# Performance work log

Hardware: AMD Instinct MI355X
Metric: run time of the kernel (lower is better)

Reference implementation:

```python
import jax, jax.numpy as jnp
import numpy as np

EPS = 1e-12  # F.normalize default eps

def _l1_normalize(x, axis):
    return x / jnp.maximum(jnp.sum(jnp.abs(x), axis=axis, keepdims=True), EPS)


def setup_inputs() -> dict:
    key = jax.random.key(0)
    k1, k2, k3, k4 = jax.random.split(key, 4)
    B_src, S_src, d = 4096, 32, 512
    B_tgt, T = 32, 256
    m = jax.random.normal(k1, (B_src, S_src, d), dtype=jnp.float32)
    om = jax.random.normal(k2, (B_tgt, T, d), dtype=jnp.float32)
    src_mask = jax.random.randint(k3, (B_src, 1, S_src), 0, 2, dtype=jnp.int32)
    tgt_mask = jax.random.randint(k4, (B_tgt, T, T), 0, 2, dtype=jnp.int32)
    return {"m": m, "om": om, "src_mask": src_mask, "tgt_mask": tgt_mask}


def reference(m, om, src_mask, tgt_mask):
    # masked mean readouts (L1-normalized masks as attention weights)
    src_w = _l1_normalize(src_mask.astype(jnp.float32), axis=-1)      # [B_src,1,S_src]
    src_readout = jnp.einsum('bos,bsd->bod', src_w, m)[:, 0, :]       # [B_src,d]
    tgt_w = _l1_normalize(tgt_mask.astype(jnp.float32), axis=-1)      # [B_tgt,T,T]
    tgt_readout = jnp.einsum('btu,bud->btd', tgt_w, om)               # [B_tgt,T,d]

    # pairwise L2 distance over d WITHOUT materializing [B_tgt,T,B_src,d]:
    # ||t - s||^2 = ||t||^2 + ||s||^2 - 2 t.s
    t_sq = jnp.sum(tgt_readout * tgt_readout, axis=-1)                # [B_tgt,T]
    s_sq = jnp.sum(src_readout * src_readout, axis=-1)                # [B_src]
    cross = jnp.einsum('btd,nd->btn', tgt_readout, src_readout)       # [B_tgt,T,B_src]
    d2 = t_sq[..., None] + s_sq[None, None, :] - 2.0 * cross
    dist = jnp.sqrt(jnp.maximum(d2, EPS))
    sim = jnp.exp(-dist)
    sim = _l1_normalize(sim, axis=-1)                                 # [B_tgt,T,B_src]
    return sim
```

## Files before the change

### kernel.cpp

```cpp
#include <hip/hip_runtime.h>
#include <math.h>

#define EPSF 1e-12f

typedef short bf16x8 __attribute__((ext_vector_type(8)));
typedef float f32x4 __attribute__((ext_vector_type(4)));

__device__ __forceinline__ void gload_lds16(const void* g, void* l) {
  __builtin_amdgcn_global_load_lds(
      (const __attribute__((address_space(1))) unsigned int*)g,
      (__attribute__((address_space(3))) unsigned int*)l, 16, 0, 0);
}

__device__ __forceinline__ unsigned short bf16_rne(float f) {
  unsigned int u = __float_as_uint(f);
  u += 0x7fffu + ((u >> 16) & 1u);
  return (unsigned short)(u >> 16);
}

__device__ __forceinline__ float bf16_to_f32(unsigned short h) {
  return __uint_as_float((unsigned int)h << 16);
}

__device__ __forceinline__ float block_reduce_sum_256(float v) {
#pragma unroll
  for (int o = 32; o > 0; o >>= 1) v += __shfl_down(v, o, 64);
  __shared__ float ws4[4];
  const int lane = threadIdx.x & 63;
  const int w = threadIdx.x >> 6;
  if (lane == 0) ws4[w] = v;
  __syncthreads();
  if (threadIdx.x == 0) ws4[0] = ws4[0] + ws4[1] + ws4[2] + ws4[3];
  __syncthreads();
  return ws4[0];
}

__global__ __launch_bounds__(256) void k_src_readout(const float* __restrict__ m,
                                                     const int* __restrict__ src_mask,
                                                     unsigned short* __restrict__ srcRb,
                                                     float* __restrict__ ssq) {
  const int tid = threadIdx.x;
  const int sub = tid >> 7, t = tid & 127;
  const int b = blockIdx.x * 2 + sub;
  __shared__ int msk[2][32];
  __shared__ float sinv[2];
  __shared__ float red[4];
  if (t < 32) msk[sub][t] = src_mask[b * 32 + t];
  __syncthreads();
  if (t == 0) {
    float c = 0.f;
    for (int s = 0; s < 32; ++s) c += (float)msk[sub][s];
    sinv[sub] = 1.0f / fmaxf(c, EPSF);
  }
  __syncthreads();
  const float inv = sinv[sub];
  const float4* mb = (const float4*)(m + (size_t)b * (32 * 512)) + t;
  float ax = 0.f, ay = 0.f, az = 0.f, aw = 0.f;
  for (int s = 0; s < 32; ++s) {
    if (msk[sub][s] != 0) {
      float4 v = mb[s * 128];
      ax += v.x; ay += v.y; az += v.z; aw += v.w;
    }
  }
  ushort4 o;
  o.x = bf16_rne(ax * inv);
  o.y = bf16_rne(ay * inv);
  o.z = bf16_rne(az * inv);
  o.w = bf16_rne(aw * inv);
  *(ushort4*)(srcRb + (size_t)b * 512 + t * 4) = o;
  float fx = bf16_to_f32(o.x), fy = bf16_to_f32(o.y);
  float fz = bf16_to_f32(o.z), fw = bf16_to_f32(o.w);
  float s = fx * fx + fy * fy + fz * fz + fw * fw;
#pragma unroll
  for (int oo = 32; oo > 0; oo >>= 1) s += __shfl_down(s, oo, 64);
  if ((tid & 63) == 0) red[tid >> 6] = s;
  __syncthreads();
  if (t == 0) ssq[b] = red[sub * 2] + red[sub * 2 + 1];
}

#define WST 72
__global__ __launch_bounds__(512) void k_tgt_readout_mfma(
    const float* __restrict__ om, const int* __restrict__ tgt_mask,
    unsigned short* __restrict__ Afrag) {
  const int b = blockIdx.x, dq = blockIdx.y, th = blockIdx.z;
  const int d0 = dq * 128, t0 = th * 128;
  __shared__ unsigned short Wb[128 * WST];
  __shared__ unsigned short omT[128 * WST];
  __shared__ float cntp[128 * 4];
  __shared__ float cnt_inv[128];
  const int tid = threadIdx.x;
  const int lane = tid & 63, w = tid >> 6;
  const int* mbase = tgt_mask + (size_t)b * 65536 + (size_t)t0 * 256;

  {
    const int t = tid >> 2, q = tid & 3;
    const int* mp = mbase + t * 256 + q * 64;
    int c = 0;
#pragma unroll
    for (int k = 0; k < 16; ++k) {
      int4 v = *(const int4*)(mp + 4 * k);
      c += v.x + v.y + v.z + v.w;
    }
    cntp[t * 4 + q] = (float)c;
  }
  __syncthreads();
  if (tid < 128) {
    float c = cntp[tid * 4] + cntp[tid * 4 + 1] + cntp[tid * 4 + 2] + cntp[tid * 4 + 3];
    cnt_inv[tid] = 1.0f / fmaxf(c, EPSF);
  }

  f32x4 acc[8];
#pragma unroll
  for (int di = 0; di < 8; ++di) acc[di] = (f32x4){0.f, 0.f, 0.f, 0.f};

  for (int uc = 0; uc < 4; ++uc) {
    const int ub = uc * 64;
    __syncthreads();
    {
      const int t = tid >> 2, ul0 = (tid & 3) * 16;
      const int* mp = mbase + t * 256 + ub + ul0;
      unsigned short* wp = Wb + t * WST + ul0;
#pragma unroll
      for (int k = 0; k < 4; ++k) {
        int4 v = *(const int4*)(mp + 4 * k);
        ushort4 h;
        h.x = v.x ? 0x3F80 : 0;
        h.y = v.y ? 0x3F80 : 0;
        h.z = v.z ? 0x3F80 : 0;
        h.w = v.w ? 0x3F80 : 0;
        *(ushort4*)(wp + 4 * k) = h;
      }
    }
    {
#pragma unroll
      for (int k = 0; k < 4; ++k) {
        const int idx = tid + 512 * k;
        const int u = idx >> 5, dl = (idx & 31) * 4;
        float4 v = *(const float4*)(om + (size_t)b * 131072 + (size_t)(ub + u) * 512 + d0 + dl);
        omT[(dl + 0) * WST + u] = bf16_rne(v.x);
        omT[(dl + 1) * WST + u] = bf16_rne(v.y);
        omT[(dl + 2) * WST + u] = bf16_rne(v.z);
        omT[(dl + 3) * WST + u] = bf16_rne(v.w);
      }
    }
    __syncthreads();
#pragma unroll
    for (int kt2 = 0; kt2 < 2; ++kt2) {
      const int ko = kt2 * 32 + (lane >> 4) * 8;
      bf16x8 wf = *(const bf16x8*)(Wb + (w * 16 + (lane & 15)) * WST + ko);
      bf16x8 of[8];
#pragma unroll
      for (int di = 0; di < 8; ++di)
        of[di] = *(const bf16x8*)(omT + (di * 16 + (lane & 15)) * WST + ko);
#pragma unroll
      for (int di = 0; di < 8; ++di)
        acc[di] = __builtin_amdgcn_mfma_f32_16x16x32_bf16(of[di], wf, acc[di], 0, 0, 0);
    }
  }

  const int tl = w * 16 + (lane & 15);
  const int rT = b * 256 + t0 + tl;
  const float inv = cnt_inv[tl];
#pragma unroll
  for (int di = 0; di < 8; ++di) {
    const int d = d0 + di * 16 + (lane >> 4) * 4;
    ushort4 o;
    o.x = bf16_rne(acc[di][0] * inv);
    o.y = bf16_rne(acc[di][1] * inv);
    o.z = bf16_rne(acc[di][2] * inv);
    o.w = bf16_rne(acc[di][3] * inv);
    const size_t off =
        (((size_t)(rT >> 4) * 16 + (d >> 5)) * 64 + ((d >> 3) & 3) * 16 + (rT & 15)) * 8 + (d & 7);
    *(ushort4*)(Afrag + off) = o;
  }
}

__global__ __launch_bounds__(256) void k_rowsq_frag(const unsigned short* __restrict__ Afrag,
                                                    float* __restrict__ sq) {
  const int r = blockIdx.x;
  const int tid = threadIdx.x;
  const int g = r >> 4, rl = r & 15;
  const int d = 2 * tid;
  const size_t off = ((size_t)((g * 16 + (d >> 5)) * 64 + ((d >> 3) & 3) * 16 + rl)) * 8 + (d & 7);
  ushort2 v = *(const ushort2*)(Afrag + off);
  float fx = bf16_to_f32(v.x), fy = bf16_to_f32(v.y);
  float s = fx * fx + fy * fy;
  s = block_reduce_sum_256(s);
  if (tid == 0) sq[r] = s;
}

template <int BF16SIM>
__global__ __launch_bounds__(512, 2) void k_cross_mfma(
    const unsigned short* __restrict__ Afrag, const unsigned short* __restrict__ B,
    const float* __restrict__ tsq, const float* __restrict__ ssq,
    unsigned short* __restrict__ simU, float* __restrict__ psum,
    float* __restrict__ outF) {
  __shared__ unsigned short Bs[128 * 512];
  const int tid = threadIdx.x;
  const int lane = tid & 63, w = tid >> 6;
  const int bid = blockIdx.x;
  const int xcd = bid & 7, idx = bid >> 3;
  const int row0 = (xcd * 2 + (idx >> 5)) * 512;
  const int col0 = (idx & 31) * 128;
  const int lr = lane & 15, lkh = lane >> 4;

#pragma unroll
  for (int t = 0; t < 16; ++t) {
    const int c = w * 16 + t;
    const int j = c >> 4, kt = c & 15;
    gload_lds16(B + (size_t)(col0 + j * 16 + lr) * 512 + kt * 32 + lkh * 8,
                Bs + (size_t)c * 512);
  }

  f32x4 acc[4][8];
#pragma unroll
  for (int i = 0; i < 4; ++i)
#pragma unroll
    for (int j = 0; j < 8; ++j) acc[i][j] = (f32x4){0.f, 0.f, 0.f, 0.f};

  __syncthreads();

  const unsigned short* ap = Afrag + ((size_t)(row0 >> 4) + w * 4) * (16 * 64 * 8);
#pragma unroll
  for (int kt = 0; kt < 16; ++kt) {
    bf16x8 af[4], bfr[8];
#pragma unroll
    for (int i = 0; i < 4; ++i)
      af[i] = *(const bf16x8*)(ap + (((size_t)i * 16 + kt) * 64 + lane) * 8);
#pragma unroll
    for (int j = 0; j < 8; ++j)
      bfr[j] = *(const bf16x8*)(Bs + ((j * 16 + kt) * 64 + lane) * 8);
#pragma unroll
    for (int i = 0; i < 4; ++i)
#pragma unroll
      for (int j = 0; j < 8; ++j)
        acc[i][j] = __builtin_amdgcn_mfma_f32_16x16x32_bf16(af[i], bfr[j], acc[i][j], 0, 0, 0);
  }

  const int cbase = col0 + (lane & 15);
  const int rbase = row0 + w * 64 + (lane >> 4) * 4;
  float ss[8];
#pragma unroll
  for (int j = 0; j < 8; ++j) ss[j] = ssq[cbase + j * 16];
#pragma unroll
  for (int i = 0; i < 4; ++i) {
#pragma unroll
    for (int r = 0; r < 4; ++r) {
      const int row = rbase + i * 16 + r;
      const float t2 = tsq[row];
      if (BF16SIM) {
        unsigned short* sp = simU + (size_t)row * 4096 + cbase;
        float s = 0.f;
#pragma unroll
        for (int j = 0; j < 8; ++j) {
          float d2 = t2 + ss[j] - 2.0f * acc[i][j][r];
          float sim = __expf(-__builtin_amdgcn_sqrtf(fmaxf(d2, EPSF)));
          s += sim;
          __builtin_nontemporal_store(bf16_rne(sim), sp + j * 16);
        }
        s += __shfl_xor(s, 1, 64);
        s += __shfl_xor(s, 2, 64);
        s += __shfl_xor(s, 4, 64);
        s += __shfl_xor(s, 8, 64);
        if ((lane & 15) == 0) psum[(size_t)(col0 >> 7) * 8192 + row] = s;
      } else {
        float* op = outF + (size_t)row * 4096 + cbase;
#pragma unroll
        for (int j = 0; j < 8; ++j) {
          float d2 = t2 + ss[j] - 2.0f * acc[i][j][r];
          float dist = __builtin_amdgcn_sqrtf(fmaxf(d2, EPSF));
          __builtin_nontemporal_store(__expf(-dist), op + j * 16);
        }
      }
    }
  }
}

__global__ __launch_bounds__(256) void k_sum_reduce(const float* __restrict__ psum,
                                                    float* __restrict__ rsinv) {
  const int row = blockIdx.x * 256 + threadIdx.x;
  float s = 0.f;
#pragma unroll
  for (int ct = 0; ct < 32; ++ct) s += psum[(size_t)ct * 8192 + row];
  rsinv[row] = 1.0f / fmaxf(s, EPSF);
}

__global__ __launch_bounds__(256) void k_scale(const unsigned short* __restrict__ simU,
                                               const float* __restrict__ rsinv,
                                               float* __restrict__ out) {
  const size_t base = (size_t)blockIdx.x * 4096;
  const float rsv = rsinv[blockIdx.x];
  const int tid = threadIdx.x;
#pragma unroll
  for (int i = 0; i < 4; ++i) {
    ushort4 v = *(const ushort4*)(simU + base + (size_t)(tid * 4 + i * 1024));
    f32x4 r;
    r[0] = bf16_to_f32(v.x) * rsv;
    r[1] = bf16_to_f32(v.y) * rsv;
    r[2] = bf16_to_f32(v.z) * rsv;
    r[3] = bf16_to_f32(v.w) * rsv;
    __builtin_nontemporal_store(r, (f32x4*)(out + base + (size_t)(tid * 4 + i * 1024)));
  }
}

__global__ __launch_bounds__(256) void k_norm(float* __restrict__ out) {
  const size_t base = (size_t)blockIdx.x * 4096;
  const int tid = threadIdx.x;
  float4 v[4];
  float s = 0.f;
#pragma unroll
  for (int i = 0; i < 4; ++i) {
    v[i] = *(const float4*)(out + base + (size_t)(tid * 4 + i * 1024));
    s += v[i].x + v[i].y + v[i].z + v[i].w;
  }
  s = block_reduce_sum_256(s);
  const float inv = 1.0f / fmaxf(s, EPSF);
#pragma unroll
  for (int i = 0; i < 4; ++i) {
    f32x4 r;
    r[0] = v[i].x * inv;
    r[1] = v[i].y * inv;
    r[2] = v[i].z * inv;
    r[3] = v[i].w * inv;
    __builtin_nontemporal_store(r, (f32x4*)(out + base + (size_t)(tid * 4 + i * 1024)));
  }
}

extern "C" void kernel_launch(void* const* d_in, const int* in_sizes, int n_in,
                              void* d_out, int out_size, void* d_ws, size_t ws_size,
                              hipStream_t stream) {
  const float* m = (const float*)d_in[0];
  const float* om = (const float*)d_in[1];
  const int* src_mask = (const int*)d_in[2];
  const int* tgt_mask = (const int*)d_in[3];
  float* out = (float*)d_out;

  float* ws = (float*)d_ws;
  float* ssq = ws;
  float* tsq = ssq + 4096;
  float* rsinv = tsq + 8192;
  float* psum = rsinv + 8192;
  unsigned short* srcRb = (unsigned short*)(psum + 32 * 8192);
  unsigned short* Afrag = srcRb + 4096 * 512;
  unsigned short* simU = Afrag + (size_t)8192 * 512;

  const size_t need = ((size_t)(4096 + 8192 + 8192) + 32 * 8192) * 4 +
                      ((size_t)4096 * 512 + (size_t)8192 * 512) * 2 +
                      (size_t)8192 * 4096 * 2;
  const bool bf16_path = ws_size >= need;

  k_src_readout<<<2048, 256, 0, stream>>>(m, src_mask, srcRb, ssq);
  k_tgt_readout_mfma<<<dim3(32, 4, 2), 512, 0, stream>>>(om, tgt_mask, Afrag);
  k_rowsq_frag<<<8192, 256, 0, stream>>>(Afrag, tsq);
  if (bf16_path) {
    k_cross_mfma<1><<<512, 512, 0, stream>>>(Afrag, srcRb, tsq, ssq, simU, psum, out);
    k_sum_reduce<<<32, 256, 0, stream>>>(psum, rsinv);
    k_scale<<<8192, 256, 0, stream>>>(simU, rsinv, out);
  } else {
    k_cross_mfma<0><<<512, 512, 0, stream>>>(Afrag, srcRb, tsq, ssq, simU, psum, out);
    k_norm<<<8192, 256, 0, stream>>>(out);
  }
}
```

Measured before the change: 150.8 us.

## Merge src/tgt readout kernels and fold row-sum reduction into scale kernel

The source and target readout kernels become one launch, with blocks split by index: 256 blocks do the tgt MFMA readout and 1024 blocks each handle four source rows. The separate psum reduction kernel is removed; psum is now stored row-major and each k_scale block reduces its own 32 partial sums before scaling. This cuts two kernel launches and lets the two independent readouts overlap, at the cost of a larger shared-memory footprint for the src blocks and a brief reduction-plus-barrier at the start of each scale block.

```diff
diff --git a/kernel.cpp b/kernel.cpp
--- a/kernel.cpp
+++ b/kernel.cpp
@@ -35,143 +35,145 @@
   return ws4[0];
 }
 
-__global__ __launch_bounds__(256) void k_src_readout(const float* __restrict__ m,
-                                                     const int* __restrict__ src_mask,
-                                                     unsigned short* __restrict__ srcRb,
-                                                     float* __restrict__ ssq) {
-  const int tid = threadIdx.x;
-  const int sub = tid >> 7, t = tid & 127;
-  const int b = blockIdx.x * 2 + sub;
-  __shared__ int msk[2][32];
-  __shared__ float sinv[2];
-  __shared__ float red[4];
-  if (t < 32) msk[sub][t] = src_mask[b * 32 + t];
-  __syncthreads();
-  if (t == 0) {
-    float c = 0.f;
-    for (int s = 0; s < 32; ++s) c += (float)msk[sub][s];
-    sinv[sub] = 1.0f / fmaxf(c, EPSF);
-  }
-  __syncthreads();
-  const float inv = sinv[sub];
-  const float4* mb = (const float4*)(m + (size_t)b * (32 * 512)) + t;
-  float ax = 0.f, ay = 0.f, az = 0.f, aw = 0.f;
-  for (int s = 0; s < 32; ++s) {
-    if (msk[sub][s] != 0) {
-      float4 v = mb[s * 128];
-      ax += v.x; ay += v.y; az += v.z; aw += v.w;
-    }
-  }
-  ushort4 o;
-  o.x = bf16_rne(ax * inv);
-  o.y = bf16_rne(ay * inv);
-  o.z = bf16_rne(az * inv);
-  o.w = bf16_rne(aw * inv);
-  *(ushort4*)(srcRb + (size_t)b * 512 + t * 4) = o;
-  float fx = bf16_to_f32(o.x), fy = bf16_to_f32(o.y);
-  float fz = bf16_to_f32(o.z), fw = bf16_to_f32(o.w);
-  float s = fx * fx + fy * fy + fz * fz + fw * fw;
-#pragma unroll
-  for (int oo = 32; oo > 0; oo >>= 1) s += __shfl_down(s, oo, 64);
-  if ((tid & 63) == 0) red[tid >> 6] = s;
-  __syncthreads();
-  if (t == 0) ssq[b] = red[sub * 2] + red[sub * 2 + 1];
-}
-
 #define WST 72
-__global__ __launch_bounds__(512) void k_tgt_readout_mfma(
+#define SMEM_BYTES 39424
+__global__ __launch_bounds__(512) void k_readouts(
+    const float* __restrict__ m, const int* __restrict__ src_mask,
+    unsigned short* __restrict__ srcRb, float* __restrict__ ssq,
     const float* __restrict__ om, const int* __restrict__ tgt_mask,
     unsigned short* __restrict__ Afrag) {
-  const int b = blockIdx.x, dq = blockIdx.y, th = blockIdx.z;
-  const int d0 = dq * 128, t0 = th * 128;
-  __shared__ unsigned short Wb[128 * WST];
-  __shared__ unsigned short omT[128 * WST];
-  __shared__ float cntp[128 * 4];
-  __shared__ float cnt_inv[128];
-  const int tid = threadIdx.x;
-  const int lane = tid & 63, w = tid >> 6;
-  const int* mbase = tgt_mask + (size_t)b * 65536 + (size_t)t0 * 256;
-
-  {
-    const int t = tid >> 2, q = tid & 3;
-    const int* mp = mbase + t * 256 + q * 64;
-    int c = 0;
-#pragma unroll
-    for (int k = 0; k < 16; ++k) {
-      int4 v = *(const int4*)(mp + 4 * k);
-      c += v.x + v.y + v.z + v.w;
-    }
-    cntp[t * 4 + q] = (float)c;
-  }
-  __syncthreads();
-  if (tid < 128) {
-    float c = cntp[tid * 4] + cntp[tid * 4 + 1] + cntp[tid * 4 + 2] + cntp[tid * 4 + 3];
-    cnt_inv[tid] = 1.0f / fmaxf(c, EPSF);
-  }
-
-  f32x4 acc[8];
-#pragma unroll
-  for (int di = 0; di < 8; ++di) acc[di] = (f32x4){0.f, 0.f, 0.f, 0.f};
-
-  for (int uc = 0; uc < 4; ++uc) {
-    const int ub = uc * 64;
+  __shared__ __attribute__((aligned(16))) char smem_raw[SMEM_BYTES];
+  const int tid = threadIdx.x;
+
+  if (blockIdx.x < 256) {
+    const int b = blockIdx.x >> 3, dq = (blockIdx.x >> 1) & 3, th = blockIdx.x & 1;
+    const int d0 = dq * 128, t0 = th * 128;
+    unsigned short* Wb = (unsigned short*)smem_raw;
+    unsigned short* omT = (unsigned short*)(smem_raw + 18432);
+    float* cntp = (float*)(smem_raw + 36864);
+    float* cnt_inv = (float*)(smem_raw + 38912);
+    const int lane = tid & 63, w = tid >> 6;
+    const int* mbase = tgt_mask + (size_t)b * 65536 + (size_t)t0 * 256;
+
+    {
+      const int t = tid >> 2, q = tid & 3;
+      const int* mp = mbase + t * 256 + q * 64;
+      int c = 0;
+#pragma unroll
+      for (int k = 0; k < 16; ++k) {
+        int4 v = *(const int4*)(mp + 4 * k);
+        c += v.x + v.y + v.z + v.w;
+      }
+      cntp[t * 4 + q] = (float)c;
+    }
     __syncthreads();
-    {
-      const int t = tid >> 2, ul0 = (tid & 3) * 16;
-      const int* mp = mbase + t * 256 + ub + ul0;
-      unsigned short* wp = Wb + t * WST + ul0;
-#pragma unroll
-      for (int k = 0; k < 4; ++k) {
-        int4 v = *(const int4*)(mp + 4 * k);
-        ushort4 h;
-        h.x = v.x ? 0x3F80 : 0;
-        h.y = v.y ? 0x3F80 : 0;
-        h.z = v.z ? 0x3F80 : 0;
-        h.w = v.w ? 0x3F80 : 0;
-        *(ushort4*)(wp + 4 * k) = h;
-      }
-    }
-    {
-#pragma unroll
-      for (int k = 0; k < 4; ++k) {
-        const int idx = tid + 512 * k;
-        const int u = idx >> 5, dl = (idx & 31) * 4;
-        float4 v = *(const float4*)(om + (size_t)b * 131072 + (size_t)(ub + u) * 512 + d0 + dl);
-        omT[(dl + 0) * WST + u] = bf16_rne(v.x);
-        omT[(dl + 1) * WST + u] = bf16_rne(v.y);
-        omT[(dl + 2) * WST + u] = bf16_rne(v.z);
-        omT[(dl + 3) * WST + u] = bf16_rne(v.w);
-      }
-    }
+    if (tid < 128) {
+      float c = cntp[tid * 4] + cntp[tid * 4 + 1] + cntp[tid * 4 + 2] + cntp[tid * 4 + 3];
+      cnt_inv[tid] = 1.0f / fmaxf(c, EPSF);
+    }
+
+    f32x4 acc[8];
+#pragma unroll
+    for (int di = 0; di < 8; ++di) acc[di] = (f32x4){0.f, 0.f, 0.f, 0.f};
+
+    for (int uc = 0; uc < 4; ++uc) {
+      const int ub = uc * 64;
+      __syncthreads();
+      {
+        const int t = tid >> 2, ul0 = (tid & 3) * 16;
+        const int* mp = mbase + t * 256 + ub + ul0;
+        unsigned short* wp = Wb + t * WST + ul0;
+#pragma unroll
+        for (int k = 0; k < 4; ++k) {
+          int4 v = *(const int4*)(mp + 4 * k);
+          ushort4 h;
+          h.x = v.x ? 0x3F80 : 0;
+          h.y = v.y ? 0x3F80 : 0;
+          h.z = v.z ? 0x3F80 : 0;
+          h.w = v.w ? 0x3F80 : 0;
+          *(ushort4*)(wp + 4 * k) = h;
+        }
+      }
+      {
+#pragma unroll
+        for (int k = 0; k < 4; ++k) {
+          const int idx = tid + 512 * k;
+          const int u = idx >> 5, dl = (idx & 31) * 4;
+          float4 v = *(const float4*)(om + (size_t)b * 131072 + (size_t)(ub + u) * 512 + d0 + dl);
+          omT[(dl + 0) * WST + u] = bf16_rne(v.x);
+          omT[(dl + 1) * WST + u] = bf16_rne(v.y);
+          omT[(dl + 2) * WST + u] = bf16_rne(v.z);
+          omT[(dl + 3) * WST + u] = bf16_rne(v.w);
+        }
+      }
+      __syncthreads();
+#pragma unroll
+      for (int kt2 = 0; kt2 < 2; ++kt2) {
+        const int ko = kt2 * 32 + (lane >> 4) * 8;
+        bf16x8 wf = *(const bf16x8*)(Wb + (w * 16 + (lane & 15)) * WST + ko);
+        bf16x8 of[8];
+#pragma unroll
+        for (int di = 0; di < 8; ++di)
+          of[di] = *(const bf16x8*)(omT + (di * 16 + (lane & 15)) * WST + ko);
+#pragma unroll
+        for (int di = 0; di < 8; ++di)
+          acc[di] = __builtin_amdgcn_mfma_f32_16x16x32_bf16(of[di], wf, acc[di], 0, 0, 0);
+      }
+    }
+
+    const int tl = w * 16 + (lane & 15);
+    const int rT = b * 256 + t0 + tl;
+    const float inv = cnt_inv[tl];
+#pragma unroll
+    for (int di = 0; di < 8; ++di) {
+      const int d = d0 + di * 16 + (lane >> 4) * 4;
+      ushort4 o;
+      o.x = bf16_rne(acc[di][0] * inv);
+      o.y = bf16_rne(acc[di][1] * inv);
+      o.z = bf16_rne(acc[di][2] * inv);
+      o.w = bf16_rne(acc[di][3] * inv);
+      const size_t off =
+          (((size_t)(rT >> 4) * 16 + (d >> 5)) * 64 + ((d >> 3) & 3) * 16 + (rT & 15)) * 8 + (d & 7);
+      *(ushort4*)(Afrag + off) = o;
+    }
+  } else {
+    const int sid = blockIdx.x - 256;
+    const int sub = tid >> 7, t = tid & 127;
+    const int b = sid * 4 + sub;
+    int* msk = (int*)smem_raw;
+    float* sinv = (float*)(smem_raw + 512);
+    float* red = (float*)(smem_raw + 528);
+    if (t < 32) msk[sub * 32 + t] = src_mask[b * 32 + t];
     __syncthreads();
-#pragma unroll
-    for (int kt2 = 0; kt2 < 2; ++kt2) {
-      const int ko = kt2 * 32 + (lane >> 4) * 8;
-      bf16x8 wf = *(const bf16x8*)(Wb + (w * 16 + (lane & 15)) * WST + ko);
-      bf16x8 of[8];
-#pragma unroll
-      for (int di = 0; di < 8; ++di)
-        of[di] = *(const bf16x8*)(omT + (di * 16 + (lane & 15)) * WST + ko);
-#pragma unroll
-      for (int di = 0; di < 8; ++di)
-        acc[di] = __builtin_amdgcn_mfma_f32_16x16x32_bf16(of[di], wf, acc[di], 0, 0, 0);
-    }
-  }
-
-  const int tl = w * 16 + (lane & 15);
-  const int rT = b * 256 + t0 + tl;
-  const float inv = cnt_inv[tl];
-#pragma unroll
-  for (int di = 0; di < 8; ++di) {
-    const int d = d0 + di * 16 + (lane >> 4) * 4;
+    if (t == 0) {
+      float c = 0.f;
+      for (int s = 0; s < 32; ++s) c += (float)msk[sub * 32 + s];
+      sinv[sub] = 1.0f / fmaxf(c, EPSF);
+    }
+    __syncthreads();
+    const float inv = sinv[sub];
+    const float4* mb = (const float4*)(m + (size_t)b * (32 * 512)) + t;
+    float ax = 0.f, ay = 0.f, az = 0.f, aw = 0.f;
+    for (int s = 0; s < 32; ++s) {
+      if (msk[sub * 32 + s] != 0) {
+        float4 v = mb[s * 128];
+        ax += v.x; ay += v.y; az += v.z; aw += v.w;
+      }
+    }
     ushort4 o;
-    o.x = bf16_rne(acc[di][0] * inv);
-    o.y = bf16_rne(acc[di][1] * inv);
-    o.z = bf16_rne(acc[di][2] * inv);
-    o.w = bf16_rne(acc[di][3] * inv);
-    const size_t off =
-        (((size_t)(rT >> 4) * 16 + (d >> 5)) * 64 + ((d >> 3) & 3) * 16 + (rT & 15)) * 8 + (d & 7);
-    *(ushort4*)(Afrag + off) = o;
+    o.x = bf16_rne(ax * inv);
+    o.y = bf16_rne(ay * inv);
+    o.z = bf16_rne(az * inv);
+    o.w = bf16_rne(aw * inv);
+    *(ushort4*)(srcRb + (size_t)b * 512 + t * 4) = o;
+    float fx = bf16_to_f32(o.x), fy = bf16_to_f32(o.y);
+    float fz = bf16_to_f32(o.z), fw = bf16_to_f32(o.w);
+    float s = fx * fx + fy * fy + fz * fz + fw * fw;
+#pragma unroll
+    for (int oo = 32; oo > 0; oo >>= 1) s += __shfl_down(s, oo, 64);
+    if ((tid & 63) == 0) red[tid >> 6] = s;
+    __syncthreads();
+    if (t == 0) ssq[b] = red[sub * 2] + red[sub * 2 + 1];
   }
 }
 
@@ -262,7 +264,7 @@
         s += __shfl_xor(s, 2, 64);
         s += __shfl_xor(s, 4, 64);
         s += __shfl_xor(s, 8, 64);
-        if ((lane & 15) == 0) psum[(size_t)(col0 >> 7) * 8192 + row] = s;
+        if ((lane & 15) == 0) psum[(size_t)row * 32 + (col0 >> 7)] = s;
       } else {
         float* op = outF + (size_t)row * 4096 + cbase;
 #pragma unroll
@@ -276,21 +278,21 @@
   }
 }
 
-__global__ __launch_bounds__(256) void k_sum_reduce(const float* __restrict__ psum,
-                                                    float* __restrict__ rsinv) {
-  const int row = blockIdx.x * 256 + threadIdx.x;
-  float s = 0.f;
-#pragma unroll
-  for (int ct = 0; ct < 32; ++ct) s += psum[(size_t)ct * 8192 + row];
-  rsinv[row] = 1.0f / fmaxf(s, EPSF);
-}
-
 __global__ __launch_bounds__(256) void k_scale(const unsigned short* __restrict__ simU,
-                                               const float* __restrict__ rsinv,
+                                               const float* __restrict__ psum,
                                                float* __restrict__ out) {
-  const size_t base = (size_t)blockIdx.x * 4096;
-  const float rsv = rsinv[blockIdx.x];
-  const int tid = threadIdx.x;
+  const int row = blockIdx.x;
+  const size_t base = (size_t)row * 4096;
+  const int tid = threadIdx.x;
+  __shared__ float srow;
+  if (tid < 32) {
+    float s = psum[(size_t)row * 32 + tid];
+#pragma unroll
+    for (int o = 16; o > 0; o >>= 1) s += __shfl_down(s, o, 64);
+    if (tid == 0) srow = 1.0f / fmaxf(s, EPSF);
+  }
+  __syncthreads();
+  const float rsv = srow;
 #pragma unroll
   for (int i = 0; i < 4; ++i) {
     ushort4 v = *(const ushort4*)(simU + base + (size_t)(tid * 4 + i * 1024));
@@ -338,24 +340,21 @@
   float* ws = (float*)d_ws;
   float* ssq = ws;
   float* tsq = ssq + 4096;
-  float* rsinv = tsq + 8192;
-  float* psum = rsinv + 8192;
+  float* psum = tsq + 8192;
   unsigned short* srcRb = (unsigned short*)(psum + 32 * 8192);
   unsigned short* Afrag = srcRb + 4096 * 512;
   unsigned short* simU = Afrag + (size_t)8192 * 512;
 
-  const size_t need = ((size_t)(4096 + 8192 + 8192) + 32 * 8192) * 4 +
+  const size_t need = ((size_t)(4096 + 8192) + 32 * 8192) * 4 +
                       ((size_t)4096 * 512 + (size_t)8192 * 512) * 2 +
                       (size_t)8192 * 4096 * 2;
   const bool bf16_path = ws_size >= need;
 
-  k_src_readout<<<2048, 256, 0, stream>>>(m, src_mask, srcRb, ssq);
-  k_tgt_readout_mfma<<<dim3(32, 4, 2), 512, 0, stream>>>(om, tgt_mask, Afrag);
+  k_readouts<<<1280, 512, 0, stream>>>(m, src_mask, srcRb, ssq, om, tgt_mask, Afrag);
   k_rowsq_frag<<<8192, 256, 0, stream>>>(Afrag, tsq);
   if (bf16_path) {
     k_cross_mfma<1><<<512, 512, 0, stream>>>(Afrag, srcRb, tsq, ssq, simU, psum, out);
-    k_sum_reduce<<<32, 256, 0, stream>>>(psum, rsinv);
-    k_scale<<<8192, 256, 0, stream>>>(simU, rsinv, out);
+    k_scale<<<8192, 256, 0, stream>>>(simU, psum, out);
   } else {
     k_cross_mfma<0><<<512, 512, 0, stream>>>(Afrag, srcRb, tsq, ssq, simU, psum, out);
     k_norm<<<8192, 256, 0, stream>>>(out);
```

Result: no change. 148.9 us (-1.3%).
